# Performance work log

Hardware: AMD Instinct MI355X
Metric: run time of the kernel (lower is better)

Reference implementation:

```python
import jax, jax.numpy as jnp
import numpy as np

B, T, H = 8, 4096, 1024   # batch, n_tokens, hidden
M, K, R = 2048, 32, 1024  # n_mentions, n_retrieval, retrieval_dim
EPS = 1e-12


def setup_inputs() -> dict:
    key = jax.random.key(0)
    ks = jax.random.split(key, 8)
    return {
        "encoded_input": jax.random.normal(ks[0], (B, T, H), dtype=jnp.float32),
        "retrieval_values": jax.random.normal(ks[1], (M, K, R), dtype=jnp.float32),
        "retrieval_scores": jax.random.uniform(ks[2], (M, K), dtype=jnp.float32),
        "W": jax.random.normal(ks[3], (R, H), dtype=jnp.float32) / np.sqrt(R),
        "b": jnp.zeros((H,), dtype=jnp.float32),
        "ln_scale": jnp.ones((H,), dtype=jnp.float32),
        "ln_bias": jnp.zeros((H,), dtype=jnp.float32),
        "mention_batch_positions": jax.random.randint(ks[4], (M,), 0, B, dtype=jnp.int32),
        "mention_start_positions": jax.random.randint(ks[5], (M,), 0, T, dtype=jnp.int32),
        "mention_end_positions": jax.random.randint(ks[6], (M,), 0, T, dtype=jnp.int32),
        "mention_mask": jax.random.randint(ks[7], (M,), 0, 2, dtype=jnp.int32),
    }


def reference(encoded_input, retrieval_values, retrieval_scores, W, b,
              ln_scale, ln_bias, mention_batch_positions,
              mention_start_positions, mention_end_positions, mention_mask):
    # Weighted sum of retrievals per mention: [M, R]
    weighted = jnp.einsum('qk,qkd->qd', retrieval_scores, retrieval_values)
    # Dense projection to hidden size, then mask padding mentions: [M, H]
    proj = (weighted @ W + b) * mention_mask.astype(weighted.dtype)[:, None]
    # Scatter-add into encoded_input at (batch_pos, start_pos)
    x = encoded_input.at[mention_batch_positions, mention_start_positions].add(proj)
    # LayerNorm over last axis (flax defaults: scale + bias)
    mean = jnp.mean(x, axis=-1, keepdims=True)
    var = jnp.mean(jnp.square(x - mean), axis=-1, keepdims=True)
    y = (x - mean) * jax.lax.rsqrt(var + EPS) * ln_scale + ln_bias
    return y
```

## Files before the change

### kernel.cpp

```cpp
#include <hip/hip_runtime.h>

#define Bb 8
#define Tt 4096
#define Hh 1024
#define Mm 2048
#define Kk 32
#define Rr 1024

__global__ __launch_bounds__(256) void k_weighted(
    const float* __restrict__ scores,
    const float* __restrict__ values,
    float* __restrict__ weighted) {
  int q = blockIdx.x;
  int t = threadIdx.x;
  __shared__ float s[Kk];
  if (t < Kk) s[t] = scores[q * Kk + t];
  __syncthreads();
  const float4* vv = (const float4*)(values + (size_t)q * Kk * Rr);
  float4 acc = make_float4(0.f, 0.f, 0.f, 0.f);
#pragma unroll 8
  for (int k = 0; k < Kk; ++k) {
    float4 v = vv[k * (Rr / 4) + t];
    float sk = s[k];
    acc.x += sk * v.x; acc.y += sk * v.y; acc.z += sk * v.z; acc.w += sk * v.w;
  }
  ((float4*)(weighted + (size_t)q * Rr))[t] = acc;
}

__global__ __launch_bounds__(256) void k_gemm(
    const float* __restrict__ A,
    const float* __restrict__ Wm,
    const float* __restrict__ bias,
    const int* __restrict__ mask,
    float* __restrict__ C) {
  __shared__ float As[16][64];
  __shared__ float Bs[16][64];
  int bn = blockIdx.x * 64;
  int bm = blockIdx.y * 64;
  int tid = threadIdx.x;
  int tx = tid & 15;
  int ty = tid >> 4;
  int arow = tid >> 2, ac4 = tid & 3;
  int brow = tid >> 4, bc4 = tid & 15;

  float acc[4][4];
#pragma unroll
  for (int i = 0; i < 4; ++i)
#pragma unroll
    for (int j = 0; j < 4; ++j) acc[i][j] = 0.f;

  for (int k0 = 0; k0 < Rr; k0 += 16) {
    float4 a = *(const float4*)(A + (size_t)(bm + arow) * Rr + k0 + ac4 * 4);
    float4 bv = *(const float4*)(Wm + (size_t)(k0 + brow) * Hh + bn + bc4 * 4);
    __syncthreads();
    As[ac4 * 4 + 0][arow] = a.x;
    As[ac4 * 4 + 1][arow] = a.y;
    As[ac4 * 4 + 2][arow] = a.z;
    As[ac4 * 4 + 3][arow] = a.w;
    *(float4*)(&Bs[brow][bc4 * 4]) = bv;
    __syncthreads();
#pragma unroll
    for (int kk = 0; kk < 16; ++kk) {
      float4 av = *(const float4*)(&As[kk][ty * 4]);
      float4 bw = *(const float4*)(&Bs[kk][tx * 4]);
      acc[0][0] += av.x * bw.x; acc[0][1] += av.x * bw.y; acc[0][2] += av.x * bw.z; acc[0][3] += av.x * bw.w;
      acc[1][0] += av.y * bw.x; acc[1][1] += av.y * bw.y; acc[1][2] += av.y * bw.z; acc[1][3] += av.y * bw.w;
      acc[2][0] += av.z * bw.x; acc[2][1] += av.z * bw.y; acc[2][2] += av.z * bw.z; acc[2][3] += av.z * bw.w;
      acc[3][0] += av.w * bw.x; acc[3][1] += av.w * bw.y; acc[3][2] += av.w * bw.z; acc[3][3] += av.w * bw.w;
    }
  }

  float4 bias4 = *(const float4*)(bias + bn + tx * 4);
#pragma unroll
  for (int i = 0; i < 4; ++i) {
    int row = bm + ty * 4 + i;
    float mk = (float)mask[row];
    float4 o;
    o.x = (acc[i][0] + bias4.x) * mk;
    o.y = (acc[i][1] + bias4.y) * mk;
    o.z = (acc[i][2] + bias4.z) * mk;
    o.w = (acc[i][3] + bias4.w) * mk;
    *(float4*)(C + (size_t)row * Hh + bn + tx * 4) = o;
  }
}

__global__ void k_init_head(int* __restrict__ head) {
  int i = blockIdx.x * 256 + threadIdx.x;
  if (i < Bb * Tt) head[i] = -1;
}

__global__ void k_link(const int* __restrict__ bpos, const int* __restrict__ spos,
                       const int* __restrict__ mask, int* __restrict__ head,
                       int* __restrict__ nxt) {
  int m = blockIdx.x * 256 + threadIdx.x;
  if (m < Mm && mask[m] != 0) {
    int row = bpos[m] * Tt + spos[m];
    nxt[m] = atomicExch(&head[row], m);
  }
}

__global__ __launch_bounds__(256) void k_ln(
    const float* __restrict__ x,
    const float* __restrict__ proj,
    const int* __restrict__ head, const int* __restrict__ nxt,
    const float* __restrict__ scale, const float* __restrict__ bias,
    float* __restrict__ out) {
  int row = blockIdx.x;
  int t = threadIdx.x;
  float4 v = ((const float4*)(x + (size_t)row * Hh))[t];
  for (int m = head[row]; m >= 0; m = nxt[m]) {
    float4 p = ((const float4*)(proj + (size_t)m * Hh))[t];
    v.x += p.x; v.y += p.y; v.z += p.z; v.w += p.w;
  }
  __shared__ float sbuf[4];
  int lane = t & 63, wave = t >> 6;

  float sum = v.x + v.y + v.z + v.w;
#pragma unroll
  for (int off = 32; off; off >>= 1) sum += __shfl_down(sum, off);
  if (lane == 0) sbuf[wave] = sum;
  __syncthreads();
  float mean = (sbuf[0] + sbuf[1] + sbuf[2] + sbuf[3]) * (1.0f / Hh);
  __syncthreads();

  float cx = v.x - mean, cy = v.y - mean, cz = v.z - mean, cw = v.w - mean;
  float ssq = cx * cx + cy * cy + cz * cz + cw * cw;
#pragma unroll
  for (int off = 32; off; off >>= 1) ssq += __shfl_down(ssq, off);
  if (lane == 0) sbuf[wave] = ssq;
  __syncthreads();
  float var = (sbuf[0] + sbuf[1] + sbuf[2] + sbuf[3]) * (1.0f / Hh);
  float inv = 1.0f / sqrtf(var + 1e-12f);

  float4 sc = ((const float4*)scale)[t];
  float4 bi = ((const float4*)bias)[t];
  float4 o;
  o.x = cx * inv * sc.x + bi.x;
  o.y = cy * inv * sc.y + bi.y;
  o.z = cz * inv * sc.z + bi.z;
  o.w = cw * inv * sc.w + bi.w;
  ((float4*)(out + (size_t)row * Hh))[t] = o;
}

extern "C" void kernel_launch(void* const* d_in, const int* in_sizes, int n_in,
                              void* d_out, int out_size, void* d_ws, size_t ws_size,
                              hipStream_t stream) {
  const float* enc      = (const float*)d_in[0];
  const float* rvals    = (const float*)d_in[1];
  const float* rscores  = (const float*)d_in[2];
  const float* Wm       = (const float*)d_in[3];
  const float* bias     = (const float*)d_in[4];
  const float* ln_scale = (const float*)d_in[5];
  const float* ln_bias  = (const float*)d_in[6];
  const int* bpos = (const int*)d_in[7];
  const int* spos = (const int*)d_in[8];
  const int* mask = (const int*)d_in[10];
  float* out = (float*)d_out;

  char* ws = (char*)d_ws;
  float* weighted = (float*)ws;
  float* proj = (float*)(ws + (size_t)Mm * Rr * 4);
  int* head = (int*)(ws + (size_t)Mm * Rr * 4 + (size_t)Mm * Hh * 4);
  int* nxt = (int*)((char*)head + (size_t)Bb * Tt * 4);

  hipLaunchKernelGGL(k_weighted, dim3(Mm), dim3(256), 0, stream,
                     rscores, rvals, weighted);
  hipLaunchKernelGGL(k_gemm, dim3(Hh / 64, Mm / 64), dim3(256), 0, stream,
                     weighted, Wm, bias, mask, proj);
  hipLaunchKernelGGL(k_init_head, dim3((Bb * Tt + 255) / 256), dim3(256), 0, stream,
                     head);
  hipLaunchKernelGGL(k_link, dim3((Mm + 255) / 256), dim3(256), 0, stream,
                     bpos, spos, mask, head, nxt);
  hipLaunchKernelGGL(k_ln, dim3(Bb * Tt), dim3(256), 0, stream,
                     enc, proj, head, nxt, ln_scale, ln_bias, out);
}
```

Before: 570.4 us.

## Restructure GEMM with register-prefetched A rows and double-buffered shared B

The projection GEMM is rebuilt with 128x64 tiles and an 8-deep k step. Each thread now loads its own 8 rows of A straight into registers (aE/aO ping-pong) instead of going through shared memory, and only W is staged through a double-buffered shared tile, leaving one barrier per step. The goal is to overlap global loads with FMA work and raise per-thread compute density. In exchange, register use grows a lot (two 8x8 A buffers plus a 32-element accumulator, with launch_bounds(256,1)), which may lower occupancy. A-row loads are also only partly coalesced across threads. The unroll factor of the weighted-sum loop is raised as well.

After: 661.2 us. 15.9% more time.

```diff
diff --git a/kernel.cpp b/kernel.cpp
--- a/kernel.cpp
+++ b/kernel.cpp
@@ -18,7 +18,7 @@
   __syncthreads();
   const float4* vv = (const float4*)(values + (size_t)q * Kk * Rr);
   float4 acc = make_float4(0.f, 0.f, 0.f, 0.f);
-#pragma unroll 8
+#pragma unroll 16
   for (int k = 0; k < Kk; ++k) {
     float4 v = vv[k * (Rr / 4) + t];
     float sk = s[k];
@@ -27,53 +27,85 @@
   ((float4*)(weighted + (size_t)q * Rr))[t] = acc;
 }
 
-__global__ __launch_bounds__(256) void k_gemm(
+#define BM 128
+#define BN 64
+#define BKk 8
+#define NSTEP (Rr / BKk)
+
+#define PREF_A(dst, k0)                                                   \
+  _Pragma("unroll") for (int i = 0; i < 8; ++i) {                         \
+    *(float4*)&dst[i][0] = *(const float4*)(Arow + (size_t)i * Rr + (k0));\
+    *(float4*)&dst[i][4] = *(const float4*)(Arow + (size_t)i * Rr + (k0) + 4);\
+  }
+
+#define LOAD_B(bv, k0)                                                    \
+  if (tid < 128) bv = *(const float4*)(Wm + (size_t)((k0) + br) * Hh + bn + bc4 * 4);
+
+#define STORE_B(buf, bv)                                                  \
+  if (tid < 128) *(float4*)(&Bs[buf][br][bc4 * 4]) = bv;
+
+#define COMPUTE(a, buf)                                                   \
+  _Pragma("unroll") for (int kk = 0; kk < BKk; ++kk) {                    \
+    float4 b = *(const float4*)(&Bs[buf][kk][tx * 4]);                    \
+    _Pragma("unroll") for (int i = 0; i < 8; ++i) {                       \
+      float av = a[i][kk];                                                \
+      acc[i][0] += av * b.x; acc[i][1] += av * b.y;                       \
+      acc[i][2] += av * b.z; acc[i][3] += av * b.w;                       \
+    }                                                                     \
+  }
+
+__global__ __launch_bounds__(256, 1) void k_gemm(
     const float* __restrict__ A,
     const float* __restrict__ Wm,
     const float* __restrict__ bias,
     const int* __restrict__ mask,
     float* __restrict__ C) {
-  __shared__ float As[16][64];
-  __shared__ float Bs[16][64];
-  int bn = blockIdx.x * 64;
-  int bm = blockIdx.y * 64;
+  __shared__ float Bs[2][BKk][BN];
   int tid = threadIdx.x;
   int tx = tid & 15;
   int ty = tid >> 4;
-  int arow = tid >> 2, ac4 = tid & 3;
-  int brow = tid >> 4, bc4 = tid & 15;
-
-  float acc[4][4];
-#pragma unroll
-  for (int i = 0; i < 4; ++i)
+  int bn = blockIdx.x * BN;
+  int bm = blockIdx.y * BM;
+  int br = tid >> 4, bc4 = tid & 15;
+  const float* Arow = A + (size_t)(bm + ty * 8) * Rr;
+
+  float acc[8][4];
+#pragma unroll
+  for (int i = 0; i < 8; ++i)
 #pragma unroll
     for (int j = 0; j < 4; ++j) acc[i][j] = 0.f;
 
-  for (int k0 = 0; k0 < Rr; k0 += 16) {
-    float4 a = *(const float4*)(A + (size_t)(bm + arow) * Rr + k0 + ac4 * 4);
-    float4 bv = *(const float4*)(Wm + (size_t)(k0 + brow) * Hh + bn + bc4 * 4);
+  float aE[8][8], aO[8][8];
+  float4 bv;
+
+  PREF_A(aE, 0)
+  LOAD_B(bv, 0)
+  STORE_B(0, bv)
+  __syncthreads();
+
+  for (int s = 0; s < NSTEP - 2; s += 2) {
+    PREF_A(aO, (s + 1) * BKk)
+    LOAD_B(bv, (s + 1) * BKk)
+    COMPUTE(aE, 0)
+    STORE_B(1, bv)
     __syncthreads();
-    As[ac4 * 4 + 0][arow] = a.x;
-    As[ac4 * 4 + 1][arow] = a.y;
-    As[ac4 * 4 + 2][arow] = a.z;
-    As[ac4 * 4 + 3][arow] = a.w;
-    *(float4*)(&Bs[brow][bc4 * 4]) = bv;
+    PREF_A(aE, (s + 2) * BKk)
+    LOAD_B(bv, (s + 2) * BKk)
+    COMPUTE(aO, 1)
+    STORE_B(0, bv)
     __syncthreads();
-#pragma unroll
-    for (int kk = 0; kk < 16; ++kk) {
-      float4 av = *(const float4*)(&As[kk][ty * 4]);
-      float4 bw = *(const float4*)(&Bs[kk][tx * 4]);
-      acc[0][0] += av.x * bw.x; acc[0][1] += av.x * bw.y; acc[0][2] += av.x * bw.z; acc[0][3] += av.x * bw.w;
-      acc[1][0] += av.y * bw.x; acc[1][1] += av.y * bw.y; acc[1][2] += av.y * bw.z; acc[1][3] += av.y * bw.w;
-      acc[2][0] += av.z * bw.x; acc[2][1] += av.z * bw.y; acc[2][2] += av.z * bw.z; acc[2][3] += av.z * bw.w;
-      acc[3][0] += av.w * bw.x; acc[3][1] += av.w * bw.y; acc[3][2] += av.w * bw.z; acc[3][3] += av.w * bw.w;
-    }
-  }
+  }
+  PREF_A(aO, (NSTEP - 1) * BKk)
+  LOAD_B(bv, (NSTEP - 1) * BKk)
+  COMPUTE(aE, 0)
+  STORE_B(1, bv)
+  __syncthreads();
+  COMPUTE(aO, 1)
 
   float4 bias4 = *(const float4*)(bias + bn + tx * 4);
 #pragma unroll
-  for (int i = 0; i < 4; ++i) {
-    int row = bm + ty * 4 + i;
+  for (int i = 0; i < 8; ++i) {
+    int row = bm + ty * 8 + i;
     float mk = (float)mask[row];
     float4 o;
     o.x = (acc[i][0] + bias4.x) * mk;
@@ -165,7 +197,7 @@
 
   hipLaunchKernelGGL(k_weighted, dim3(Mm), dim3(256), 0, stream,
                      rscores, rvals, weighted);
-  hipLaunchKernelGGL(k_gemm, dim3(Hh / 64, Mm / 64), dim3(256), 0, stream,
+  hipLaunchKernelGGL(k_gemm, dim3(Hh / BN, Mm / BM), dim3(256), 0, stream,
                      weighted, Wm, bias, mask, proj);
   hipLaunchKernelGGL(k_init_head, dim3((Bb * Tt + 255) / 256), dim3(256), 0, stream,
                      head);
```
